# Optimization experiments

Measured on AMD Instinct MI355X. Metric: run time of the kernel, lower is better.

Reference implementation:

```python
import jax, jax.numpy as jnp
import numpy as np

NEG_INF = -1e15  # matches masked_fill value -1000000000000000.0
ALPHA = 0.2      # leakyReLU negative slope


def setup_inputs() -> dict:
    key = jax.random.key(0)
    k1, k2, k3, k4 = jax.random.split(key, 4)
    N, F_IN, F_OUT = 8192, 256, 64
    x = jax.random.normal(k1, (N, F_IN), dtype=jnp.float32)
    mask = jax.random.randint(k2, (N, N), 0, 2, dtype=jnp.int32)
    trans = jax.random.normal(k3, (F_IN, F_OUT), dtype=jnp.float32) * 0.1
    attn = jax.random.normal(k4, (2 * F_OUT, 1), dtype=jnp.float32) * 0.1
    return {"x": x, "mask": mask, "trans": trans, "attn": attn}


def reference(x, mask, trans, attn):
    d = trans.shape[1]
    h = x @ trans                                  # [N, d]
    e1 = h @ attn[:d, :]                           # [N, 1]
    e2 = h @ attn[d:, :]                           # [N, 1]
    scores = jax.nn.leaky_relu(e1 + e2.T, negative_slope=ALPHA)  # [N, N]
    masked = jnp.where(mask == 0, NEG_INF, scores)
    attention = jax.nn.softmax(masked, axis=1)
    return attention @ h                           # [N, d]
```

## Files before the change

kernel.cpp:

```cpp
#include <hip/hip_runtime.h>
#include <hip/hip_bf16.h>
#include <math.h>

#define N 8192
#define FIN 256
#define D 64
#define ALPHA 0.2f

typedef __attribute__((ext_vector_type(8))) short bf16x8;
typedef __attribute__((ext_vector_type(4))) float f32x4;

__global__ __launch_bounds__(256) void k_pack(
    const int* __restrict__ mask, unsigned char* __restrict__ mp)
{
    const size_t t = (size_t)blockIdx.x * 256 + threadIdx.x;
    const int4* s = (const int4*)mask + 2 * t;
    const int4 a = s[0], b = s[1];
    unsigned v = (a.x != 0 ? 1u : 0u) | (a.y != 0 ? 2u : 0u)
               | (a.z != 0 ? 4u : 0u) | (a.w != 0 ? 8u : 0u)
               | (b.x != 0 ? 16u : 0u) | (b.y != 0 ? 32u : 0u)
               | (b.z != 0 ? 64u : 0u) | (b.w != 0 ? 128u : 0u);
    mp[t] = (unsigned char)v;
}

__global__ __launch_bounds__(256) void k_h_e(
    const float* __restrict__ x, const float* __restrict__ trans,
    const float* __restrict__ attn,
    __hip_bfloat16* __restrict__ hT, float* __restrict__ e1, float* __restrict__ e2)
{
    __shared__ float xs[8 * FIN];
    __shared__ __hip_bfloat16 hl[8 * D];
    const int t = threadIdx.x;
    const int r0 = blockIdx.x * 8;

    #pragma unroll
    for (int v = 0; v < 2; ++v) {
        int idx = t + 256 * v;
        ((float4*)xs)[idx] = ((const float4*)(x + (size_t)r0 * FIN))[idx];
    }
    __syncthreads();

    const int lane = t & 63, w = t >> 6;
    const float* xa = xs + (2 * w) * FIN;
    const float* xb = xs + (2 * w + 1) * FIN;
    float acca = 0.f, accb = 0.f;
    #pragma unroll 8
    for (int k = 0; k < FIN; ++k) {
        const float tv = trans[k * D + lane];
        acca = fmaf(xa[k], tv, acca);
        accb = fmaf(xb[k], tv, accb);
    }
    const int ra = r0 + 2 * w, rb = ra + 1;

    const float a1 = attn[lane], a2 = attn[D + lane];
    float p1a = acca * a1, p2a = acca * a2;
    float p1b = accb * a1, p2b = accb * a2;
    #pragma unroll
    for (int mm = 1; mm <= 32; mm <<= 1) {
        p1a += __shfl_xor(p1a, mm);
        p2a += __shfl_xor(p2a, mm);
        p1b += __shfl_xor(p1b, mm);
        p2b += __shfl_xor(p2b, mm);
    }
    if (lane == 0) { e1[ra] = p1a; e2[ra] = p2a; e1[rb] = p1b; e2[rb] = p2b; }

    hl[(2 * w) * D + lane]     = __float2bfloat16(acca);
    hl[(2 * w + 1) * D + lane] = __float2bfloat16(accb);
    __syncthreads();
    if (t < D) {
        union { bf16x8 v; __hip_bfloat16 h[8]; } o;
        #pragma unroll
        for (int r = 0; r < 8; ++r) o.h[r] = hl[r * D + t];
        *(bf16x8*)(hT + (size_t)t * N + r0) = o.v;
    }
}

__global__ __launch_bounds__(256) void k_attn(
    const unsigned char* __restrict__ mp, const __hip_bfloat16* __restrict__ hT,
    const float* __restrict__ e1, const float* __restrict__ e2,
    float* __restrict__ acc_part, float* __restrict__ l_part, int cs)
{
    const int t = threadIdx.x;
    const int lane = t & 63, wave = t >> 6;
    const int i0 = (blockIdx.y * 4 + wave) * 16;
    const int sp = blockIdx.x;
    const int c0 = sp * cs;
    const int m = lane & 15, quad = lane >> 4;
    const int row = i0 + m;
    const float er = e1[row];

    const unsigned char* mb = mp + ((size_t)row << 10) + (c0 >> 3) + quad;

    f32x4 acc0 = {0.f, 0.f, 0.f, 0.f};
    f32x4 acc1 = {0.f, 0.f, 0.f, 0.f};
    f32x4 acc2 = {0.f, 0.f, 0.f, 0.f};
    f32x4 acc3 = {0.f, 0.f, 0.f, 0.f};
    float lsum = 0.f;

    const __hip_bfloat16* hb0 = hT + (size_t)(m     ) * N;
    const __hip_bfloat16* hb1 = hT + (size_t)(m + 16) * N;
    const __hip_bfloat16* hb2 = hT + (size_t)(m + 32) * N;
    const __hip_bfloat16* hb3 = hT + (size_t)(m + 48) * N;

    const int jb0 = c0 + quad * 8;
    const int iters = cs >> 5;

    unsigned mc = mb[0];
    float4 ea = *(const float4*)(e2 + jb0);
    float4 eb = *(const float4*)(e2 + jb0 + 4);
    bf16x8 b0 = *(const bf16x8*)(hb0 + jb0);
    bf16x8 b1 = *(const bf16x8*)(hb1 + jb0);
    bf16x8 b2 = *(const bf16x8*)(hb2 + jb0);
    bf16x8 b3 = *(const bf16x8*)(hb3 + jb0);

    for (int it = 0; it < iters; ++it) {
        const int jn = jb0 + (it + 1) * 32;
        const unsigned mn = mb[(it + 1) * 4];
        const float4 na = *(const float4*)(e2 + jn);
        const float4 nb = *(const float4*)(e2 + jn + 4);
        const bf16x8 n0 = *(const bf16x8*)(hb0 + jn);
        const bf16x8 n1 = *(const bf16x8*)(hb1 + jn);
        const bf16x8 n2 = *(const bf16x8*)(hb2 + jn);
        const bf16x8 n3 = *(const bf16x8*)(hb3 + jn);

        float s0 = er + ea.x; s0 = s0 > 0.f ? s0 : ALPHA * s0;
        float s1 = er + ea.y; s1 = s1 > 0.f ? s1 : ALPHA * s1;
        float s2 = er + ea.z; s2 = s2 > 0.f ? s2 : ALPHA * s2;
        float s3 = er + ea.w; s3 = s3 > 0.f ? s3 : ALPHA * s3;
        float s4 = er + eb.x; s4 = s4 > 0.f ? s4 : ALPHA * s4;
        float s5 = er + eb.y; s5 = s5 > 0.f ? s5 : ALPHA * s5;
        float s6 = er + eb.z; s6 = s6 > 0.f ? s6 : ALPHA * s6;
        float s7 = er + eb.w; s7 = s7 > 0.f ? s7 : ALPHA * s7;
        const float p0 = (mc & 1u)   ? __expf(s0) : 0.f;
        const float p1 = (mc & 2u)   ? __expf(s1) : 0.f;
        const float p2 = (mc & 4u)   ? __expf(s2) : 0.f;
        const float p3 = (mc & 8u)   ? __expf(s3) : 0.f;
        const float p4 = (mc & 16u)  ? __expf(s4) : 0.f;
        const float p5 = (mc & 32u)  ? __expf(s5) : 0.f;
        const float p6 = (mc & 64u)  ? __expf(s6) : 0.f;
        const float p7 = (mc & 128u) ? __expf(s7) : 0.f;

        union { bf16x8 v; __hip_bfloat162 h2[4]; } af;
        af.h2[0] = __float22bfloat162_rn(make_float2(p0, p1));
        af.h2[1] = __float22bfloat162_rn(make_float2(p2, p3));
        af.h2[2] = __float22bfloat162_rn(make_float2(p4, p5));
        af.h2[3] = __float22bfloat162_rn(make_float2(p6, p7));

        lsum += ((p0 + p1) + (p2 + p3)) + ((p4 + p5) + (p6 + p7));

        acc0 = __builtin_amdgcn_mfma_f32_16x16x32_bf16(af.v, b0, acc0, 0, 0, 0);
        acc1 = __builtin_amdgcn_mfma_f32_16x16x32_bf16(af.v, b1, acc1, 0, 0, 0);
        acc2 = __builtin_amdgcn_mfma_f32_16x16x32_bf16(af.v, b2, acc2, 0, 0, 0);
        acc3 = __builtin_amdgcn_mfma_f32_16x16x32_bf16(af.v, b3, acc3, 0, 0, 0);

        mc = mn; ea = na; eb = nb; b0 = n0; b1 = n1; b2 = n2; b3 = n3;
    }

    lsum += __shfl_xor(lsum, 16);
    lsum += __shfl_xor(lsum, 32);
    if (quad == 0) l_part[(size_t)sp * N + row] = lsum;

    #pragma unroll
    for (int reg = 0; reg < 4; ++reg) {
        const size_t rbase = ((size_t)sp * N + i0 + quad * 4 + reg) * D;
        acc_part[rbase + m     ] = acc0[reg];
        acc_part[rbase + m + 16] = acc1[reg];
        acc_part[rbase + m + 32] = acc2[reg];
        acc_part[rbase + m + 48] = acc3[reg];
    }
}

__global__ __launch_bounds__(256) void k_reduce(
    const float* __restrict__ acc_part, const float* __restrict__ l_part,
    float* __restrict__ out, int nsplit)
{
    const int idx = blockIdx.x * 256 + threadIdx.x;
    const int row = idx >> 6;
    float sum = 0.f, l = 0.f;
    for (int s = 0; s < nsplit; ++s) {
        sum += acc_part[(size_t)s * N * D + idx];
        l   += l_part[(size_t)s * N + row];
    }
    out[idx] = sum / l;
}

extern "C" void kernel_launch(void* const* d_in, const int* in_sizes, int n_in,
                              void* d_out, int out_size, void* d_ws, size_t ws_size,
                              hipStream_t stream) {
    const float* x     = (const float*)d_in[0];
    const int*   mask  = (const int*)d_in[1];
    const float* trans = (const float*)d_in[2];
    const float* attn  = (const float*)d_in[3];
    float* out = (float*)d_out;

    char* ws = (char*)d_ws;
    __hip_bfloat16* hT = (__hip_bfloat16*)ws;
    char* p = ws + (size_t)D * N * sizeof(__hip_bfloat16);
    float* e1 = (float*)p;            p += (size_t)N * sizeof(float);
    float* e2 = (float*)p;            p += (size_t)N * sizeof(float);
    unsigned char* mp = (unsigned char*)p;  p += (size_t)N * (N / 8);
    const size_t used = (size_t)(p - ws);
    int nsplit = 1;
    const int cands[4] = {8, 4, 2, 1};
    for (int ci = 0; ci < 4; ++ci) {
        int s = cands[ci];
        size_t need = used + (size_t)s * N * sizeof(float)
                    + (size_t)s * N * D * sizeof(float) + 4096;
        if (need <= ws_size) { nsplit = s; break; }
    }
    float* l_part = (float*)p;
    float* acc_part = l_part + (size_t)nsplit * N;

    k_pack<<<(N / 16) * (N / 128), 256, 0, stream>>>(mask, mp);
    k_h_e<<<N / 8, 256, 0, stream>>>(x, trans, attn, hT, e1, e2);
    dim3 g2(nsplit, N / 64);
    k_attn<<<g2, 256, 0, stream>>>(mp, hT, e1, e2, acc_part, l_part, N / nsplit);
    k_reduce<<<(N * D) / 256, 256, 0, stream>>>(acc_part, l_part, out, nsplit);
}
```

Measured before the change: 461.7 us.

## Store packed mask and h in MFMA fragment order for coalesced loads

The packed mask and the bf16 h matrix are now written in a fragment-ordered layout, so each lane in the attention kernel reads contiguous bytes (one mask byte per lane, consecutive bf16x8 per lane) instead of strided rows. The pack kernel is restructured to loop over half a row-tile per block and write into this tiled layout. The manual register double-buffering in the attention loop is removed and left to the compiler. The split-count selection loop is also rewritten slightly. The risk is lost prefetch overlap and a less parallel pack kernel with scattered byte stores.

```diff
diff --git a/kernel.cpp b/kernel.cpp
--- a/kernel.cpp
+++ b/kernel.cpp
@@ -11,22 +11,32 @@
 typedef __attribute__((ext_vector_type(4))) float f32x4;
 
 __global__ __launch_bounds__(256) void k_pack(
-    const int* __restrict__ mask, unsigned char* __restrict__ mp)
-{
-    const size_t t = (size_t)blockIdx.x * 256 + threadIdx.x;
-    const int4* s = (const int4*)mask + 2 * t;
-    const int4 a = s[0], b = s[1];
-    unsigned v = (a.x != 0 ? 1u : 0u) | (a.y != 0 ? 2u : 0u)
-               | (a.z != 0 ? 4u : 0u) | (a.w != 0 ? 8u : 0u)
-               | (b.x != 0 ? 16u : 0u) | (b.y != 0 ? 32u : 0u)
-               | (b.z != 0 ? 64u : 0u) | (b.w != 0 ? 128u : 0u);
-    mp[t] = (unsigned char)v;
+    const int* __restrict__ mask, unsigned char* __restrict__ mF)
+{
+    const int t = threadIdx.x;
+    const int rt = blockIdx.x >> 1;
+    const int half = blockIdx.x & 1;
+    const int row = rt * 16 + (t >> 4);
+    const int c = t & 15;
+    const int m = t >> 4;
+    for (int cc = half * (N / 2); cc < (half + 1) * (N / 2); cc += 128) {
+        const int col = cc + c * 8;
+        const int4 a = *(const int4*)(mask + (size_t)row * N + col);
+        const int4 b = *(const int4*)(mask + (size_t)row * N + col + 4);
+        unsigned v = (a.x != 0 ? 1u : 0u) | (a.y != 0 ? 2u : 0u)
+                   | (a.z != 0 ? 4u : 0u) | (a.w != 0 ? 8u : 0u)
+                   | (b.x != 0 ? 16u : 0u) | (b.y != 0 ? 32u : 0u)
+                   | (b.z != 0 ? 64u : 0u) | (b.w != 0 ? 128u : 0u);
+        const int cb = col >> 5;
+        const int jgrp = c & 3;
+        mF[((size_t)rt * 256 + cb) * 64 + jgrp * 16 + m] = (unsigned char)v;
+    }
 }
 
 __global__ __launch_bounds__(256) void k_h_e(
     const float* __restrict__ x, const float* __restrict__ trans,
     const float* __restrict__ attn,
-    __hip_bfloat16* __restrict__ hT, float* __restrict__ e1, float* __restrict__ e2)
+    __hip_bfloat16* __restrict__ hF, float* __restrict__ e1, float* __restrict__ e2)
 {
     __shared__ float xs[8 * FIN];
     __shared__ __hip_bfloat16 hl[8 * D];
@@ -68,28 +78,32 @@
     hl[(2 * w + 1) * D + lane] = __float2bfloat16(accb);
     __syncthreads();
     if (t < D) {
+        const int q = t >> 4, m = t & 15;
+        const int cb = r0 >> 5, jgrp = (r0 >> 3) & 3;
         union { bf16x8 v; __hip_bfloat16 h[8]; } o;
         #pragma unroll
-        for (int r = 0; r < 8; ++r) o.h[r] = hl[r * D + t];
-        *(bf16x8*)(hT + (size_t)t * N + r0) = o.v;
+        for (int r = 0; r < 8; ++r) o.h[r] = hl[r * D + q * 16 + m];
+        *(bf16x8*)(hF + (((size_t)cb * 4 + q) * 64 + jgrp * 16 + m) * 8) = o.v;
     }
 }
 
 __global__ __launch_bounds__(256) void k_attn(
-    const unsigned char* __restrict__ mp, const __hip_bfloat16* __restrict__ hT,
+    const unsigned char* __restrict__ mF, const __hip_bfloat16* __restrict__ hF,
     const float* __restrict__ e1, const float* __restrict__ e2,
     float* __restrict__ acc_part, float* __restrict__ l_part, int cs)
 {
     const int t = threadIdx.x;
     const int lane = t & 63, wave = t >> 6;
     const int i0 = (blockIdx.y * 4 + wave) * 16;
+    const int rt = blockIdx.y * 4 + wave;
     const int sp = blockIdx.x;
     const int c0 = sp * cs;
     const int m = lane & 15, quad = lane >> 4;
     const int row = i0 + m;
     const float er = e1[row];
 
-    const unsigned char* mb = mp + ((size_t)row << 10) + (c0 >> 3) + quad;
+    const unsigned char* mbp = mF + ((size_t)rt * 256 + (c0 >> 5)) * 64 + lane;
+    const __hip_bfloat16* hfp = hF + (((size_t)(c0 >> 5)) * 4 * 64 + lane) * 8;
 
     f32x4 acc0 = {0.f, 0.f, 0.f, 0.f};
     f32x4 acc1 = {0.f, 0.f, 0.f, 0.f};
@@ -97,31 +111,17 @@
     f32x4 acc3 = {0.f, 0.f, 0.f, 0.f};
     float lsum = 0.f;
 
-    const __hip_bfloat16* hb0 = hT + (size_t)(m     ) * N;
-    const __hip_bfloat16* hb1 = hT + (size_t)(m + 16) * N;
-    const __hip_bfloat16* hb2 = hT + (size_t)(m + 32) * N;
-    const __hip_bfloat16* hb3 = hT + (size_t)(m + 48) * N;
-
-    const int jb0 = c0 + quad * 8;
     const int iters = cs >> 5;
-
-    unsigned mc = mb[0];
-    float4 ea = *(const float4*)(e2 + jb0);
-    float4 eb = *(const float4*)(e2 + jb0 + 4);
-    bf16x8 b0 = *(const bf16x8*)(hb0 + jb0);
-    bf16x8 b1 = *(const bf16x8*)(hb1 + jb0);
-    bf16x8 b2 = *(const bf16x8*)(hb2 + jb0);
-    bf16x8 b3 = *(const bf16x8*)(hb3 + jb0);
-
     for (int it = 0; it < iters; ++it) {
-        const int jn = jb0 + (it + 1) * 32;
-        const unsigned mn = mb[(it + 1) * 4];
-        const float4 na = *(const float4*)(e2 + jn);
-        const float4 nb = *(const float4*)(e2 + jn + 4);
-        const bf16x8 n0 = *(const bf16x8*)(hb0 + jn);
-        const bf16x8 n1 = *(const bf16x8*)(hb1 + jn);
-        const bf16x8 n2 = *(const bf16x8*)(hb2 + jn);
-        const bf16x8 n3 = *(const bf16x8*)(hb3 + jn);
+        const int jb = c0 + it * 32 + quad * 8;
+        const unsigned mc = mbp[it * 64];
+        const float4 ea = *(const float4*)(e2 + jb);
+        const float4 eb = *(const float4*)(e2 + jb + 4);
+        const bf16x8* hq = (const bf16x8*)(hfp + (size_t)it * 2048);
+        const bf16x8 b0 = hq[0];
+        const bf16x8 b1 = hq[64];
+        const bf16x8 b2 = hq[128];
+        const bf16x8 b3 = hq[192];
 
         float s0 = er + ea.x; s0 = s0 > 0.f ? s0 : ALPHA * s0;
         float s1 = er + ea.y; s1 = s1 > 0.f ? s1 : ALPHA * s1;
@@ -152,8 +152,6 @@
         acc1 = __builtin_amdgcn_mfma_f32_16x16x32_bf16(af.v, b1, acc1, 0, 0, 0);
         acc2 = __builtin_amdgcn_mfma_f32_16x16x32_bf16(af.v, b2, acc2, 0, 0, 0);
         acc3 = __builtin_amdgcn_mfma_f32_16x16x32_bf16(af.v, b3, acc3, 0, 0, 0);
-
-        mc = mn; ea = na; eb = nb; b0 = n0; b1 = n1; b2 = n2; b3 = n3;
     }
 
     lsum += __shfl_xor(lsum, 16);
@@ -194,26 +192,26 @@
     float* out = (float*)d_out;
 
     char* ws = (char*)d_ws;
-    __hip_bfloat16* hT = (__hip_bfloat16*)ws;
+    __hip_bfloat16* hF = (__hip_bfloat16*)ws;
     char* p = ws + (size_t)D * N * sizeof(__hip_bfloat16);
     float* e1 = (float*)p;            p += (size_t)N * sizeof(float);
     float* e2 = (float*)p;            p += (size_t)N * sizeof(float);
-    unsigned char* mp = (unsigned char*)p;  p += (size_t)N * (N / 8);
+    unsigned char* mF = (unsigned char*)p;  p += (size_t)N * (N / 8);
+
     const size_t used = (size_t)(p - ws);
-    int nsplit = 1;
-    const int cands[4] = {8, 4, 2, 1};
-    for (int ci = 0; ci < 4; ++ci) {
-        int s = cands[ci];
-        size_t need = used + (size_t)s * N * sizeof(float)
-                    + (size_t)s * N * D * sizeof(float) + 4096;
-        if (need <= ws_size) { nsplit = s; break; }
+    int nsplit = 8;
+    while (nsplit > 1) {
+        size_t need = used + (size_t)nsplit * N * sizeof(float)
+                    + (size_t)nsplit * N * D * sizeof(float);
+        if (need <= ws_size) break;
+        nsplit >>= 1;
     }
     float* l_part = (float*)p;
     float* acc_part = l_part + (size_t)nsplit * N;
 
-    k_pack<<<(N / 16) * (N / 128), 256, 0, stream>>>(mask, mp);
-    k_h_e<<<N / 8, 256, 0, stream>>>(x, trans, attn, hT, e1, e2);
+    k_pack<<<(N / 16) * 2, 256, 0, stream>>>(mask, mF);
+    k_h_e<<<N / 8, 256, 0, stream>>>(x, trans, attn, hF, e1, e2);
     dim3 g2(nsplit, N / 64);
-    k_attn<<<g2, 256, 0, stream>>>(mp, hT, e1, e2, acc_part, l_part, N / nsplit);
+    k_attn<<<g2, 256, 0, stream>>>(mF, hF, e1, e2, acc_part, l_part, N / nsplit);
     k_reduce<<<(N * D) / 256, 256, 0, stream>>>(acc_part, l_part, out, nsplit);
 }
```

Result: faster. 427.7 us (-7.4%).
